# Optimization experiments

Hardware: AMD Instinct MI355X
Metric: run time of the kernel (lower is better)

Reference implementation:

```python
import jax, jax.numpy as jnp
import numpy as np

D_MODEL = 1024
N_HEADS = 16
N_KV_HEADS = 4
HEAD_DIM = 64


def setup_inputs() -> dict:
    key = jax.random.key(0)
    ks = jax.random.split(key, 5)
    B, T, P = 2, 512, 8
    scale = 1.0 / np.sqrt(D_MODEL)
    return {
        "hidden_states": jax.random.normal(ks[0], (B, T, P, D_MODEL), dtype=jnp.float32),
        # weights stored [in, out] so y = x @ W (same math as nn.Linear with W^T)
        "Wq": jax.random.normal(ks[1], (D_MODEL, N_HEADS * HEAD_DIM), dtype=jnp.float32) * scale,
        "Wk": jax.random.normal(ks[2], (D_MODEL, N_KV_HEADS * HEAD_DIM), dtype=jnp.float32) * scale,
        "Wv": jax.random.normal(ks[3], (D_MODEL, N_KV_HEADS * HEAD_DIM), dtype=jnp.float32) * scale,
        "Wo": jax.random.normal(ks[4], (N_HEADS * HEAD_DIM, D_MODEL), dtype=jnp.float32) * scale,
    }


def _rope_tables(T, d):
    half = d // 2
    inv_freq = 1.0 / (10000.0 ** (jnp.arange(half, dtype=jnp.float32) / half))
    pos = jnp.arange(T, dtype=jnp.float32)
    angles = pos[:, None] * inv_freq[None, :]  # (T, half)
    return jnp.cos(angles), jnp.sin(angles)


def _apply_rope(x, cos, sin):
    # x: (B, P, T, H, d); cos/sin: (T, d/2)
    half = x.shape[-1] // 2
    x1, x2 = x[..., :half], x[..., half:]
    c = cos[None, None, :, None, :]
    s = sin[None, None, :, None, :]
    return jnp.concatenate([x1 * c - x2 * s, x1 * s + x2 * c], axis=-1)


def reference(hidden_states, Wq, Wk, Wv, Wo):
    B, T, P, _ = hidden_states.shape
    x = jnp.transpose(hidden_states, (0, 2, 1, 3))  # (B, P, T, C)
    q = (x @ Wq).reshape(B, P, T, N_HEADS, HEAD_DIM)
    k = (x @ Wk).reshape(B, P, T, N_KV_HEADS, HEAD_DIM)
    v = (x @ Wv).reshape(B, P, T, N_KV_HEADS, HEAD_DIM)

    rep = N_HEADS // N_KV_HEADS
    k = jnp.repeat(k, rep, axis=3)  # (B,P,T,H,d) interleaved like torch repeat/view
    v = jnp.repeat(v, rep, axis=3)

    cos, sin = _rope_tables(T, HEAD_DIM)
    q = _apply_rope(q, cos, sin)
    k = _apply_rope(k, cos, sin)

    # (B,P,H,T,d)
    q = jnp.transpose(q, (0, 1, 3, 2, 4))
    k = jnp.transpose(k, (0, 1, 3, 2, 4))
    v = jnp.transpose(v, (0, 1, 3, 2, 4))

    attn = jnp.einsum("bphqd,bphkd->bphqk", q, k) / jnp.sqrt(
        jnp.asarray(HEAD_DIM, q.dtype))
    attn = jax.nn.softmax(attn, axis=-1)
    out = jnp.einsum("bphqk,bphkd->bphqd", attn, v)
    out = jnp.transpose(out, (0, 1, 3, 2, 4)).reshape(B, P, T, N_HEADS * HEAD_DIM)
    out = jnp.transpose(out, (0, 2, 1, 3))  # (B, T, P, H*d)
    return out @ Wo
```

## Files before the change

### kernel.cpp

```cpp
#include <hip/hip_runtime.h>
#include <stdint.h>


typedef __attribute__((ext_vector_type(8))) short bf16x8;
typedef __attribute__((ext_vector_type(4))) float f32x4;
typedef __attribute__((ext_vector_type(16))) float f32x16;
typedef __attribute__((ext_vector_type(4))) unsigned short us4;
typedef __attribute__((ext_vector_type(8))) unsigned short us8;

static __device__ __forceinline__ unsigned short f2bf(float f) {
  unsigned u = __float_as_uint(f);
  u += 0x7fffu + ((u >> 16) & 1u);
  return (unsigned short)(u >> 16);
}

static __device__ __forceinline__ void ld_lds16(const void* g, void* l) {
  __builtin_amdgcn_global_load_lds(
      (const __attribute__((address_space(1))) void*)g,
      (__attribute__((address_space(3))) void*)l, 16, 0, 0);
}

static __device__ __forceinline__ f32x4 mfma16(bf16x8 a, bf16x8 b, f32x4 c) {
  return __builtin_amdgcn_mfma_f32_16x16x32_bf16(a, b, c, 0, 0, 0);
}
static __device__ __forceinline__ f32x16 mfma32(bf16x8 a, bf16x8 b, f32x16 c) {
  return __builtin_amdgcn_mfma_f32_32x32x16_bf16(a, b, c, 0, 0, 0);
}

__global__ __launch_bounds__(256) void conv_all(
    const float* __restrict__ hs, const float* __restrict__ Wq,
    const float* __restrict__ Wk, const float* __restrict__ Wv,
    const float* __restrict__ Wo, unsigned short* __restrict__ xb,
    unsigned short* __restrict__ wqkv, unsigned short* __restrict__ wot) {
  __shared__ float tile[64][65];
  int bid = blockIdx.x, tid = threadIdx.x;
  if (bid < 8192) {
    int gid = bid * 256 + tid;
    size_t e = (size_t)gid * 4;
    int r = (int)(e >> 10);
    int d = (int)(e & 1023);
    int b = r >> 12, p = (r >> 9) & 7, t = r & 511;
    const float4* src = (const float4*)(hs + ((((size_t)b * 512 + t) * 8 + p) << 10) + d);
    float4 v = *src;
    us4 o;
    o.x = f2bf(v.x); o.y = f2bf(v.y); o.z = f2bf(v.z); o.w = f2bf(v.w);
    *(us4*)(xb + e) = o;
    return;
  }
  int tb = bid - 8192;
  const float* W; unsigned short* Wt; int N, tc0, tn0;
  if (tb < 256)      { W = Wq; Wt = wqkv;                       N = 1024; tc0 = (tb >> 4) * 64;          tn0 = (tb & 15) * 64; }
  else if (tb < 320) { W = Wk; Wt = wqkv + (size_t)1024 * 1024; N = 256;  tc0 = ((tb - 256) >> 2) * 64;  tn0 = ((tb - 256) & 3) * 64; }
  else if (tb < 384) { W = Wv; Wt = wqkv + (size_t)1280 * 1024; N = 256;  tc0 = ((tb - 320) >> 2) * 64;  tn0 = ((tb - 320) & 3) * 64; }
  else               { W = Wo; Wt = wot;                        N = 1024; tc0 = ((tb - 384) >> 4) * 64;  tn0 = ((tb - 384) & 15) * 64; }
  int tr = tid >> 4, tc = tid & 15;
#pragma unroll
  for (int i = 0; i < 4; ++i) {
    int c = tr + i * 16;
    float4 v = *(const float4*)(W + (size_t)(tc0 + c) * N + tn0 + tc * 4);
    tile[c][tc * 4 + 0] = v.x; tile[c][tc * 4 + 1] = v.y;
    tile[c][tc * 4 + 2] = v.z; tile[c][tc * 4 + 3] = v.w;
  }
  __syncthreads();
#pragma unroll
  for (int i = 0; i < 4; ++i) {
    int n = tr + i * 16;
    us4 o;
    o.x = f2bf(tile[tc * 4 + 0][n]); o.y = f2bf(tile[tc * 4 + 1][n]);
    o.z = f2bf(tile[tc * 4 + 2][n]); o.w = f2bf(tile[tc * 4 + 3][n]);
    *(us4*)(Wt + (size_t)(tn0 + n) * 1024 + tc0 + tc * 4) = o;
  }
}

template <int NT, int MODE>
__global__ __launch_bounds__(256, 3) void gemm_bt(
    const unsigned short* __restrict__ A, const unsigned short* __restrict__ Bt,
    unsigned short* __restrict__ qb, unsigned short* __restrict__ kb,
    unsigned short* __restrict__ vtb, float* __restrict__ out) {
  constexpr int K = 1024;
  __shared__ __align__(16) unsigned short Sm[128 * 128];
  unsigned short* As = Sm;
  unsigned short* Bs = Sm + 128 * 64;
  unsigned short* Cs = Sm;

  int tid = threadIdx.x;
  int lane = tid & 63, wid = tid >> 6;
  int quad = lane >> 4, lo = lane & 15;
  int tn = blockIdx.x % NT, tm = blockIdx.x / NT;
  int wm = (wid >> 1) * 64, wn = (wid & 1) * 64;
  int srow = lane >> 3, schunk = lane & 7;

  f32x4 z = {0.f, 0.f, 0.f, 0.f};
  f32x4 acc[4][4];
  for (int i = 0; i < 4; ++i) for (int j = 0; j < 4; ++j) acc[i][j] = z;

  int cg = schunk ^ srow;
  const unsigned short* pa = A + ((size_t)(tm * 128) + wid * 8 + srow) * K + cg * 8;
  const unsigned short* pb = Bt + ((size_t)(tn * 128) + wid * 8 + srow) * K + cg * 8;
  unsigned short* wA = As + (size_t)(wid * 8 + srow * 0) * 0;
  char* dA = (char*)As + (wid * 8) * 128 + lane * 16;
  char* dB = (char*)Bs + (wid * 8) * 128 + lane * 16;

  us8 ra[4], rb[4];
#pragma unroll
  for (int i = 0; i < 4; ++i) {
    ra[i] = *(const us8*)(pa + (size_t)i * 32 * K);
    rb[i] = *(const us8*)(pb + (size_t)i * 32 * K);
  }

  for (int k0 = 0; k0 < K; k0 += 64) {
    __syncthreads();
#pragma unroll
    for (int i = 0; i < 4; ++i) {
      *(us8*)(dA + i * 32 * 128) = ra[i];
      *(us8*)(dB + i * 32 * 128) = rb[i];
    }
    __syncthreads();
    if (k0 + 64 < K) {
#pragma unroll
      for (int i = 0; i < 4; ++i) {
        ra[i] = *(const us8*)(pa + (size_t)i * 32 * K + k0 + 64);
        rb[i] = *(const us8*)(pb + (size_t)i * 32 * K + k0 + 64);
      }
    }
#pragma unroll
    for (int kk = 0; kk < 64; kk += 32) {
      bf16x8 af[4], bb[4];
#pragma unroll
      for (int mi = 0; mi < 4; ++mi) {
        int row = wm + mi * 16 + lo;
        int cgx = (quad + (kk >> 3)) ^ (row & 7);
        af[mi] = *(const bf16x8*)(As + (size_t)row * 64 + cgx * 8);
      }
#pragma unroll
      for (int ni = 0; ni < 4; ++ni) {
        int row = wn + ni * 16 + lo;
        int cgx = (quad + (kk >> 3)) ^ (row & 7);
        bb[ni] = *(const bf16x8*)(Bs + (size_t)row * 64 + cgx * 8);
      }
#pragma unroll
      for (int mi = 0; mi < 4; ++mi)
#pragma unroll
        for (int ni = 0; ni < 4; ++ni)
          acc[mi][ni] = mfma16(af[mi], bb[ni], acc[mi][ni]);
    }
  }

  __syncthreads();

  if (MODE == 0 && tn < 10) {
    float qscale = (tn < 8) ? 0.125f : 1.0f;
#pragma unroll
    for (int mi = 0; mi < 4; ++mi)
#pragma unroll
      for (int r = 0; r < 4; ++r) {
        int t = (tm * 128 + wm + mi * 16 + quad * 4 + r) & 511;
#pragma unroll
        for (int ni = 0; ni < 2; ++ni) {
          float inv = exp2f((float)(ni * 16 + lo) * -0.41524101186092029f);
          float ang = (float)t * inv;
          float s, c;
          __sincosf(ang, &s, &c);
          float x1 = acc[mi][ni][r], x2 = acc[mi][ni + 2][r];
          acc[mi][ni][r]     = (x1 * c - x2 * s) * qscale;
          acc[mi][ni + 2][r] = (x1 * s + x2 * c) * qscale;
        }
      }
#pragma unroll
    for (int mi = 0; mi < 4; ++mi)
#pragma unroll
      for (int ni = 0; ni < 4; ++ni)
#pragma unroll
        for (int r = 0; r < 4; ++r) {
          int row = wm + mi * 16 + quad * 4 + r;
          int col = wn + ni * 16 + lo;
          int cs = col ^ (((row >> 2) & 3) << 3);
          Cs[row * 128 + cs] = f2bf(acc[mi][ni][r]);
        }
    __syncthreads();
    int tc = tid & 15, ro = tid >> 4;
#pragma unroll
    for (int it = 0; it < 8; ++it) {
      int row = ro + 16 * it;
      int cs = (tc * 8) ^ (((row >> 2) & 3) << 3);
      us8 v = *(const us8*)(Cs + row * 128 + cs);
      size_t grow = (size_t)(tm * 128 + row);
      if (tn < 8) {
        *(us8*)(qb + grow * 1024 + tn * 128 + tc * 8) = v;
      } else {
        *(us8*)(kb + grow * 256 + (tn - 8) * 128 + tc * 8) = v;
      }
    }
  } else {
    for (int mi = 0; mi < 4; ++mi) {
      for (int ni = 0; ni < 4; ++ni) {
        int col = tn * 128 + wn + ni * 16 + lo;
        for (int r = 0; r < 4; ++r) {
          int grow = tm * 128 + wm + mi * 16 + quad * 4 + r;
          float val = acc[mi][ni][r];
          if (MODE == 0) {
            int cc = col - 1280;
            int hh = cc >> 6, dd = cc & 63;
            int bp = grow >> 9, t = grow & 511;
            vtb[(((size_t)(bp * 4 + hh)) * 64 + dd) * 512 + t] = f2bf(val);
          } else {
            int bp = grow >> 9, t = grow & 511;
            int b = bp >> 3, p = bp & 7;
            out[((((size_t)b * 512 + t) * 8 + p) << 10) + col] = val;
          }
        }
      }
    }
  }
}

__global__ __launch_bounds__(256, 4) void attn(
    const unsigned short* __restrict__ qb, const unsigned short* __restrict__ kb,
    const unsigned short* __restrict__ vtb, unsigned short* __restrict__ ao) {
  __shared__ __align__(16) unsigned short Qs[128 * 64];
  __shared__ __align__(16) unsigned short Ks[64 * 64];
  __shared__ __align__(16) unsigned short Vs[64 * 64];

  int tid = threadIdx.x;
  int lane = tid & 63, wid = tid >> 6;
  int lo32 = lane & 31, hl = lane >> 5;
  int qt = blockIdx.x & 3, bph = blockIdx.x >> 2;
  int head = bph & 15, bp = bph >> 4;
  int kvh = head >> 2;
  int t0 = qt * 128;
  int srow = lane >> 3, schunk = lane & 7;

  const unsigned short* qg = qb + ((size_t)(bp * 512 + t0)) * 1024 + head * 64;
  const unsigned short* kg = kb + ((size_t)bp * 512) * 256 + kvh * 64;
  const unsigned short* vg = vtb + ((size_t)(bp * 4 + kvh)) * 64 * 512;

  for (int i = 0; i < 4; ++i) {
    int row = wid * 8 + i * 32 + srow;
    int cg = schunk ^ (row & 7);
    ld_lds16(qg + (size_t)row * 1024 + cg * 8, (char*)Qs + (wid * 8 + i * 32) * 128);
  }

  f32x16 z16 = {0.f};
  f32x16 o0 = z16, o1 = z16;
  float psum = 0.f;
  int qrow = wid * 32 + lo32;

  for (int kt = 0; kt < 512; kt += 64) {
    __syncthreads();
    for (int i = 0; i < 2; ++i) {
      int row = wid * 8 + i * 32 + srow;
      int cg = schunk ^ (row & 7);
      ld_lds16(kg + (size_t)(kt + row) * 256 + cg * 8, (char*)Ks + (wid * 8 + i * 32) * 128);
      ld_lds16(vg + (size_t)row * 512 + kt + cg * 8, (char*)Vs + (wid * 8 + i * 32) * 128);
    }
    __syncthreads();

    f32x16 st0 = z16, st1 = z16;
#pragma unroll
    for (int kkc = 0; kkc < 4; ++kkc) {
      int ch = 2 * kkc + hl;
      bf16x8 qf = *(const bf16x8*)(Qs + (size_t)qrow * 64 + ((ch ^ (qrow & 7)) * 8));
      bf16x8 kf0 = *(const bf16x8*)(Ks + (size_t)lo32 * 64 + ((ch ^ (lo32 & 7)) * 8));
      bf16x8 kf1 = *(const bf16x8*)(Ks + (size_t)(32 + lo32) * 64 + ((ch ^ (lo32 & 7)) * 8));
      st0 = mfma32(kf0, qf, st0);
      st1 = mfma32(kf1, qf, st1);
    }

#pragma unroll
    for (int t = 0; t < 2; ++t) {
      const f32x16& stv = t ? st1 : st0;
      unsigned pk[8], xpk[8];
#pragma unroll
      for (int p = 0; p < 8; ++p) {
        float e0 = __expf(stv[2 * p]);
        float e1 = __expf(stv[2 * p + 1]);
        psum += e0 + e1;
        pk[p] = ((__float_as_uint(e0) + 0x8000u) >> 16) |
                ((__float_as_uint(e1) + 0x8000u) & 0xffff0000u);
      }
#pragma unroll
      for (int p = 0; p < 8; ++p) xpk[p] = (unsigned)__shfl_xor((int)pk[p], 32);
#pragma unroll
      for (int cc = 0; cc < 2; ++cc) {
        int o = cc * 4;
        union { unsigned u[4]; bf16x8 v; } af;
        if (hl == 0) {
          af.u[0] = pk[o];      af.u[1] = pk[o + 1];
          af.u[2] = xpk[o];     af.u[3] = xpk[o + 1];
        } else {
          af.u[0] = xpk[o + 2]; af.u[1] = xpk[o + 3];
          af.u[2] = pk[o + 2];  af.u[3] = pk[o + 3];
        }
        int vch = 2 * (t * 2 + cc) + hl;
        bf16x8 v0 = *(const bf16x8*)(Vs + (size_t)lo32 * 64 + ((vch ^ (lo32 & 7)) * 8));
        bf16x8 v1 = *(const bf16x8*)(Vs + (size_t)(32 + lo32) * 64 + ((vch ^ (lo32 & 7)) * 8));
        o0 = mfma32(af.v, v0, o0);
        o1 = mfma32(af.v, v1, o1);
      }
    }
  }

  psum += __shfl_xor(psum, 32);
  float inv = 1.f / psum;
#pragma unroll
  for (int r = 0; r < 16; ++r) {
    int q_r = (r & 3) + 8 * (r >> 2) + 4 * hl;
    float sc = __shfl(inv, q_r);
    size_t grow = (size_t)(bp * 512 + t0 + wid * 32 + q_r);
    ao[grow * 1024 + head * 64 + lo32]      = f2bf(o0[r] * sc);
    ao[grow * 1024 + head * 64 + 32 + lo32] = f2bf(o1[r] * sc);
  }
}

extern "C" void kernel_launch(void* const* d_in, const int* in_sizes, int n_in,
                              void* d_out, int out_size, void* d_ws, size_t ws_size,
                              hipStream_t stream) {
  const float* hs = (const float*)d_in[0];
  const float* Wq = (const float*)d_in[1];
  const float* Wk = (const float*)d_in[2];
  const float* Wv = (const float*)d_in[3];
  const float* Wo = (const float*)d_in[4];
  float* out = (float*)d_out;

  unsigned short* xb   = (unsigned short*)d_ws;
  unsigned short* wqkv = xb + (size_t)8192 * 1024;
  unsigned short* wot  = wqkv + (size_t)1536 * 1024;
  unsigned short* qbuf = wot + (size_t)1024 * 1024;
  unsigned short* kbuf = qbuf + (size_t)8192 * 1024;
  unsigned short* vtb  = kbuf + (size_t)8192 * 256;
  unsigned short* ao   = xb;

  conv_all<<<8832, 256, 0, stream>>>(hs, Wq, Wk, Wv, Wo, xb, wqkv, wot);
  gemm_bt<12, 0><<<768, 256, 0, stream>>>(xb, wqkv, qbuf, kbuf, vtb, nullptr);
  attn<<<1024, 256, 0, stream>>>(qbuf, kbuf, vtb, ao);
  gemm_bt<8, 1><<<512, 256, 0, stream>>>(ao, wot, nullptr, nullptr, nullptr, out);
}
```

Baseline: 176.3 us.

## Fuse activation fp32-to-bf16 conversion into QKV GEMM and register-prefetch attention K/V

```diff
diff --git a/kernel.cpp b/kernel.cpp
--- a/kernel.cpp
+++ b/kernel.cpp
@@ -1,4 +1,5 @@
 #include <hip/hip_runtime.h>
+#include <hip/hip_bf16.h>
 #include <stdint.h>
 
 
@@ -14,6 +15,15 @@
   return (unsigned short)(u >> 16);
 }
 
+static __device__ __forceinline__ us8 pack8(float4 a, float4 b) {
+  union { __hip_bfloat162 h[4]; us8 v; } u;
+  u.h[0] = __float22bfloat162_rn(make_float2(a.x, a.y));
+  u.h[1] = __float22bfloat162_rn(make_float2(a.z, a.w));
+  u.h[2] = __float22bfloat162_rn(make_float2(b.x, b.y));
+  u.h[3] = __float22bfloat162_rn(make_float2(b.z, b.w));
+  return u.v;
+}
+
 static __device__ __forceinline__ void ld_lds16(const void* g, void* l) {
   __builtin_amdgcn_global_load_lds(
       (const __attribute__((address_space(1))) void*)g,
@@ -27,27 +37,12 @@
   return __builtin_amdgcn_mfma_f32_32x32x16_bf16(a, b, c, 0, 0, 0);
 }
 
-__global__ __launch_bounds__(256) void conv_all(
-    const float* __restrict__ hs, const float* __restrict__ Wq,
-    const float* __restrict__ Wk, const float* __restrict__ Wv,
-    const float* __restrict__ Wo, unsigned short* __restrict__ xb,
+__global__ __launch_bounds__(256) void conv_w(
+    const float* __restrict__ Wq, const float* __restrict__ Wk,
+    const float* __restrict__ Wv, const float* __restrict__ Wo,
     unsigned short* __restrict__ wqkv, unsigned short* __restrict__ wot) {
   __shared__ float tile[64][65];
-  int bid = blockIdx.x, tid = threadIdx.x;
-  if (bid < 8192) {
-    int gid = bid * 256 + tid;
-    size_t e = (size_t)gid * 4;
-    int r = (int)(e >> 10);
-    int d = (int)(e & 1023);
-    int b = r >> 12, p = (r >> 9) & 7, t = r & 511;
-    const float4* src = (const float4*)(hs + ((((size_t)b * 512 + t) * 8 + p) << 10) + d);
-    float4 v = *src;
-    us4 o;
-    o.x = f2bf(v.x); o.y = f2bf(v.y); o.z = f2bf(v.z); o.w = f2bf(v.w);
-    *(us4*)(xb + e) = o;
-    return;
-  }
-  int tb = bid - 8192;
+  int tb = blockIdx.x, tid = threadIdx.x;
   const float* W; unsigned short* Wt; int N, tc0, tn0;
   if (tb < 256)      { W = Wq; Wt = wqkv;                       N = 1024; tc0 = (tb >> 4) * 64;          tn0 = (tb & 15) * 64; }
   else if (tb < 320) { W = Wk; Wt = wqkv + (size_t)1024 * 1024; N = 256;  tc0 = ((tb - 256) >> 2) * 64;  tn0 = ((tb - 256) & 3) * 64; }
@@ -74,7 +69,8 @@
 
 template <int NT, int MODE>
 __global__ __launch_bounds__(256, 3) void gemm_bt(
-    const unsigned short* __restrict__ A, const unsigned short* __restrict__ Bt,
+    const float* __restrict__ Af, const unsigned short* __restrict__ A,
+    const unsigned short* __restrict__ Bt,
     unsigned short* __restrict__ qb, unsigned short* __restrict__ kb,
     unsigned short* __restrict__ vtb, float* __restrict__ out) {
   constexpr int K = 1024;
@@ -86,7 +82,7 @@
   int tid = threadIdx.x;
   int lane = tid & 63, wid = tid >> 6;
   int quad = lane >> 4, lo = lane & 15;
-  int tn = blockIdx.x % NT, tm = blockIdx.x / NT;
+  int tm = blockIdx.x & 63, tn = blockIdx.x >> 6;
   int wm = (wid >> 1) * 64, wn = (wid & 1) * 64;
   int srow = lane >> 3, schunk = lane & 7;
 
@@ -95,16 +91,30 @@
   for (int i = 0; i < 4; ++i) for (int j = 0; j < 4; ++j) acc[i][j] = z;
 
   int cg = schunk ^ srow;
-  const unsigned short* pa = A + ((size_t)(tm * 128) + wid * 8 + srow) * K + cg * 8;
-  const unsigned short* pb = Bt + ((size_t)(tn * 128) + wid * 8 + srow) * K + cg * 8;
-  unsigned short* wA = As + (size_t)(wid * 8 + srow * 0) * 0;
+  int rowl = wid * 8 + srow;
+  const unsigned short* pb = Bt + ((size_t)(tn * 128) + rowl) * K + cg * 8;
   char* dA = (char*)As + (wid * 8) * 128 + lane * 16;
   char* dB = (char*)Bs + (wid * 8) * 128 + lane * 16;
 
+  const float* pax = nullptr;
+  const unsigned short* pa = nullptr;
+  if constexpr (MODE == 0) {
+    int bp = tm >> 2, tt = tm & 3, b = bp >> 3, p = bp & 7;
+    pax = Af + ((size_t)b * 4096 + (size_t)(tt * 128 + rowl) * 8 + p) * 1024 + cg * 8;
+  } else {
+    pa = A + ((size_t)(tm * 128) + rowl) * K + cg * 8;
+  }
+
+  float4 raf[8];
   us8 ra[4], rb[4];
 #pragma unroll
   for (int i = 0; i < 4; ++i) {
-    ra[i] = *(const us8*)(pa + (size_t)i * 32 * K);
+    if constexpr (MODE == 0) {
+      raf[2 * i]     = *(const float4*)(pax + (size_t)i * 32 * 8192);
+      raf[2 * i + 1] = *(const float4*)(pax + (size_t)i * 32 * 8192 + 4);
+    } else {
+      ra[i] = *(const us8*)(pa + (size_t)i * 32 * K);
+    }
     rb[i] = *(const us8*)(pb + (size_t)i * 32 * K);
   }
 
@@ -112,14 +122,23 @@
     __syncthreads();
 #pragma unroll
     for (int i = 0; i < 4; ++i) {
-      *(us8*)(dA + i * 32 * 128) = ra[i];
+      if constexpr (MODE == 0) {
+        *(us8*)(dA + i * 32 * 128) = pack8(raf[2 * i], raf[2 * i + 1]);
+      } else {
+        *(us8*)(dA + i * 32 * 128) = ra[i];
+      }
       *(us8*)(dB + i * 32 * 128) = rb[i];
     }
     __syncthreads();
     if (k0 + 64 < K) {
 #pragma unroll
       for (int i = 0; i < 4; ++i) {
-        ra[i] = *(const us8*)(pa + (size_t)i * 32 * K + k0 + 64);
+        if constexpr (MODE == 0) {
+          raf[2 * i]     = *(const float4*)(pax + (size_t)i * 32 * 8192 + k0 + 64);
+          raf[2 * i + 1] = *(const float4*)(pax + (size_t)i * 32 * 8192 + k0 + 68);
+        } else {
+          ra[i] = *(const us8*)(pa + (size_t)i * 32 * K + k0 + 64);
+        }
         rb[i] = *(const us8*)(pb + (size_t)i * 32 * K + k0 + 64);
       }
     }
@@ -236,9 +255,20 @@
 
   for (int i = 0; i < 4; ++i) {
     int row = wid * 8 + i * 32 + srow;
-    int cg = schunk ^ (row & 7);
-    ld_lds16(qg + (size_t)row * 1024 + cg * 8, (char*)Qs + (wid * 8 + i * 32) * 128);
-  }
+    int cgq = schunk ^ (row & 7);
+    ld_lds16(qg + (size_t)row * 1024 + cgq * 8, (char*)Qs + (wid * 8 + i * 32) * 128);
+  }
+
+  int cg = schunk ^ srow;
+  int row0 = wid * 8 + srow, row1 = row0 + 32;
+  char* dK = (char*)Ks + (wid * 8) * 128 + lane * 16;
+  char* dV = (char*)Vs + (wid * 8) * 128 + lane * 16;
+
+  us8 rk[2], rv[2];
+  rk[0] = *(const us8*)(kg + (size_t)row0 * 256 + cg * 8);
+  rk[1] = *(const us8*)(kg + (size_t)row1 * 256 + cg * 8);
+  rv[0] = *(const us8*)(vg + (size_t)row0 * 512 + cg * 8);
+  rv[1] = *(const us8*)(vg + (size_t)row1 * 512 + cg * 8);
 
   f32x16 z16 = {0.f};
   f32x16 o0 = z16, o1 = z16;
@@ -247,13 +277,15 @@
 
   for (int kt = 0; kt < 512; kt += 64) {
     __syncthreads();
-    for (int i = 0; i < 2; ++i) {
-      int row = wid * 8 + i * 32 + srow;
-      int cg = schunk ^ (row & 7);
-      ld_lds16(kg + (size_t)(kt + row) * 256 + cg * 8, (char*)Ks + (wid * 8 + i * 32) * 128);
-      ld_lds16(vg + (size_t)row * 512 + kt + cg * 8, (char*)Vs + (wid * 8 + i * 32) * 128);
-    }
-    __syncthreads();
+    *(us8*)(dK) = rk[0];  *(us8*)(dK + 32 * 128) = rk[1];
+    *(us8*)(dV) = rv[0];  *(us8*)(dV + 32 * 128) = rv[1];
+    __syncthreads();
+    if (kt + 64 < 512) {
+      rk[0] = *(const us8*)(kg + (size_t)(kt + 64 + row0) * 256 + cg * 8);
+      rk[1] = *(const us8*)(kg + (size_t)(kt + 64 + row1) * 256 + cg * 8);
+      rv[0] = *(const us8*)(vg + (size_t)row0 * 512 + kt + 64 + cg * 8);
+      rv[1] = *(const us8*)(vg + (size_t)row1 * 512 + kt + 64 + cg * 8);
+    }
 
     f32x16 st0 = z16, st1 = z16;
 #pragma unroll
@@ -322,16 +354,15 @@
   const float* Wo = (const float*)d_in[4];
   float* out = (float*)d_out;
 
-  unsigned short* xb   = (unsigned short*)d_ws;
-  unsigned short* wqkv = xb + (size_t)8192 * 1024;
+  unsigned short* wqkv = (unsigned short*)d_ws;
   unsigned short* wot  = wqkv + (size_t)1536 * 1024;
   unsigned short* qbuf = wot + (size_t)1024 * 1024;
   unsigned short* kbuf = qbuf + (size_t)8192 * 1024;
   unsigned short* vtb  = kbuf + (size_t)8192 * 256;
-  unsigned short* ao   = xb;
-
-  conv_all<<<8832, 256, 0, stream>>>(hs, Wq, Wk, Wv, Wo, xb, wqkv, wot);
-  gemm_bt<12, 0><<<768, 256, 0, stream>>>(xb, wqkv, qbuf, kbuf, vtb, nullptr);
+  unsigned short* ao   = vtb + (size_t)8192 * 256;
+
+  conv_w<<<640, 256, 0, stream>>>(Wq, Wk, Wv, Wo, wqkv, wot);
+  gemm_bt<12, 0><<<768, 256, 0, stream>>>(hs, nullptr, wqkv, qbuf, kbuf, vtb, nullptr);
   attn<<<1024, 256, 0, stream>>>(qbuf, kbuf, vtb, ao);
-  gemm_bt<8, 1><<<512, 256, 0, stream>>>(ao, wot, nullptr, nullptr, nullptr, out);
-}
+  gemm_bt<8, 1><<<512, 256, 0, stream>>>(nullptr, ao, wot, nullptr, nullptr, nullptr, out);
+}
```

Result: slower. 183.9 us (+4.3%).
